# Optimization experiments

Measured on AMD Instinct MI355X. Metric: run time of the kernel, lower is better.

Reference implementation:

```python
import jax, jax.numpy as jnp
import numpy as np

K_HEADS = 8
D_HEAD = 64
D = K_HEADS * D_HEAD  # 512
B, TP, TQ, N = 8, 48, 48, 256


def setup_inputs() -> dict:
    key = jax.random.key(0)
    ks = jax.random.split(key, 13)
    s = 1.0 / np.sqrt(D)
    inp = {
        "X": jax.random.normal(ks[0], (B, TP, N, D), jnp.float32),
        "STE_P": jax.random.normal(ks[1], (B, TP, N, D), jnp.float32),
        "STE_Q": jax.random.normal(ks[2], (B, TQ, N, D), jnp.float32),
        "Wq": jax.random.uniform(ks[3], (D, D), jnp.float32, -s, s),
        "bq": jax.random.uniform(ks[4], (D,), jnp.float32, -s, s),
        "Wk": jax.random.uniform(ks[5], (D, D), jnp.float32, -s, s),
        "bk": jax.random.uniform(ks[6], (D,), jnp.float32, -s, s),
        "Wv": jax.random.uniform(ks[7], (D, D), jnp.float32, -s, s),
        "bv": jax.random.uniform(ks[8], (D,), jnp.float32, -s, s),
        "W1": jax.random.uniform(ks[9], (D, D), jnp.float32, -s, s),
        "b1": jax.random.uniform(ks[10], (D,), jnp.float32, -s, s),
        "W2": jax.random.uniform(ks[11], (D, D), jnp.float32, -s, s),
        "b2": jax.random.uniform(ks[12], (D,), jnp.float32, -s, s),
    }
    return inp


def reference(X, STE_P, STE_Q, Wq, bq, Wk, bk, Wv, bv, W1, b1, W2, b2):
    # ReLU-fused QKV projections
    q = jax.nn.relu(STE_Q @ Wq + bq)  # [B, Tq, N, D]
    k = jax.nn.relu(STE_P @ Wk + bk)  # [B, Tp, N, D]
    v = jax.nn.relu(X @ Wv + bv)      # [B, Tp, N, D]

    # split(last, d) + cat(dim 0) == introduce head axis h of size K
    b, tq, n, _ = q.shape
    tp = k.shape[1]
    q = q.reshape(b, tq, n, K_HEADS, D_HEAD)
    k = k.reshape(b, tp, n, K_HEADS, D_HEAD)
    v = v.reshape(b, tp, n, K_HEADS, D_HEAD)

    # attention over the TIME axis, per node and head: scores [b,h,n,tq,tp]
    scale = 1.0 / jnp.sqrt(jnp.asarray(D_HEAD, q.dtype))
    attn = jnp.einsum('bqnhd,bpnhd->bhnqp', q, k) * scale
    attn = jax.nn.softmax(attn, axis=-1)
    out = jnp.einsum('bhnqp,bpnhd->bqnhd', attn, v).reshape(b, tq, n, D)

    out = jax.nn.relu(out @ W1 + b1) @ W2 + b2
    return out
```

## Files before the change

kernel.cpp:

```cpp
#include <hip/hip_runtime.h>

typedef _Float16 f16;
typedef __fp16 hf2 __attribute__((ext_vector_type(2)));
typedef _Float16 f16x4 __attribute__((ext_vector_type(4)));
typedef _Float16 f16x8 __attribute__((ext_vector_type(8)));
typedef float f32x4 __attribute__((ext_vector_type(4)));

typedef const __attribute__((address_space(1))) unsigned int guint;
typedef __attribute__((address_space(3))) unsigned int luint;
__device__ __forceinline__ void gl_lds16(const void* g, void* l) {
    __builtin_amdgcn_global_load_lds((guint*)g, (luint*)l, 16, 0, 0);
}
template <int N>
__device__ __forceinline__ void vmwait() {
    if constexpr (N == 8)       asm volatile("s_waitcnt vmcnt(8)" ::: "memory");
    else if constexpr (N == 4)  asm volatile("s_waitcnt vmcnt(4)" ::: "memory");
    else                        asm volatile("s_waitcnt vmcnt(0)" ::: "memory");
}
__device__ __forceinline__ void barrier_raw() { __builtin_amdgcn_s_barrier(); __builtin_amdgcn_sched_barrier(0); }

__global__ __launch_bounds__(256) void wconv(const float* w0, const float* w1, const float* w2,
                                             const float* w3, const float* w4, f16* dst) {
    const float* src;
    switch (blockIdx.z) { case 0: src = w0; break; case 1: src = w1; break;
                          case 2: src = w2; break; case 3: src = w3; break; default: src = w4; }
    __shared__ float tile[32][33];
    int k0 = blockIdx.x * 32, n0 = blockIdx.y * 32;
    int t = threadIdx.x;
    int r = t >> 3, c4 = (t & 7) * 4;
    float4 v = *(const float4*)(src + (k0 + r) * 512 + n0 + c4);
    tile[r][c4 + 0] = v.x; tile[r][c4 + 1] = v.y; tile[r][c4 + 2] = v.z; tile[r][c4 + 3] = v.w;
    __syncthreads();
    f16x4 o;
    o[0] = (f16)tile[c4 + 0][r]; o[1] = (f16)tile[c4 + 1][r];
    o[2] = (f16)tile[c4 + 2][r]; o[3] = (f16)tile[c4 + 3][r];
    *(f16x4*)(dst + (size_t)blockIdx.z * 262144 + (n0 + r) * 512 + k0 + c4) = o;
}

template <bool A16, bool RELU, bool O16>
__global__ __launch_bounds__(512) void gemm_w8(const void* __restrict__ Ap,
                                               const f16* __restrict__ Bt,
                                               const float* __restrict__ bias,
                                               void* __restrict__ Cp) {
    constexpr int ASZ = A16 ? 16384 : 32768;
    constexpr int BSZ = 8192;
    constexpr int BUF = ASZ + BSZ;
    __shared__ __align__(16) char smem[2 * BUF];

    const int cpx = gridDim.x >> 3;
    const int orig = blockIdx.x;
    const int wgid = (orig & 7) * cpx + (orig >> 3);
    const int by = wgid & 3;
    const int bx = wgid >> 2;
    const int r0 = bx * 256, c0 = by * 128;

    const int t = threadIdx.x;
    const int j = t & 63, w = t >> 6;
    const int lr = j & 15, lq = j >> 4;
    const int wr = (w >> 1) * 64, wc = (w & 1) * 64;

    const char* aSrc;
    if (A16) aSrc = (const char*)Ap + ((size_t)(r0 + (t >> 2)) * 512 + ((t & 3) ^ ((t >> 3) & 3)) * 8) * 2;
    else     aSrc = (const char*)Ap + ((size_t)(r0 + (t >> 3)) * 512 + ((t & 7) ^ ((t >> 3) & 7)) * 4) * 4;
    const char* bSrc = (const char*)Bt + ((size_t)(c0 + (t >> 2)) * 512 + ((t & 3) ^ ((t >> 3) & 3)) * 8) * 2;

    int aoffL[4], aoffH[4], boff[4];
#pragma unroll
    for (int m = 0; m < 4; m++) {
        int row = wr + m * 16 + lr;
        if (A16) {
            aoffL[m] = row * 64 + ((lq ^ ((row >> 1) & 3)) << 4);
        } else {
            int s = row & 7;
            aoffL[m] = row * 128 + (((2 * lq) ^ s) << 4);
            aoffH[m] = row * 128 + (((2 * lq + 1) ^ s) << 4);
        }
    }
#pragma unroll
    for (int nb = 0; nb < 4; nb++) {
        int row = wc + nb * 16 + lr;
        boff[nb] = ASZ + row * 64 + ((lq ^ ((row >> 1) & 3)) << 4);
    }

    f32x4 acc[4][4] = {};

#define STAGE(tk, buf)                                                     \
    do {                                                                   \
        char* al_ = smem + (buf) * BUF + t * 16;                           \
        if (A16) {                                                         \
            const char* as_ = aSrc + (size_t)(tk) * 64;                    \
            gl_lds16(as_, al_);                                            \
            gl_lds16(as_ + 131072, al_ + 8192);                            \
        } else {                                                           \
            const char* as_ = aSrc + (size_t)(tk) * 128;                   \
            gl_lds16(as_, al_);                                            \
            gl_lds16(as_ + 131072, al_ + 8192);                            \
            gl_lds16(as_ + 262144, al_ + 16384);                           \
            gl_lds16(as_ + 393216, al_ + 24576);                           \
        }                                                                  \
        const char* bs_ = bSrc + (size_t)(tk) * 64;                        \
        gl_lds16(bs_, smem + (buf) * BUF + ASZ + t * 16);                  \
    } while (0)

#define COMPUTE(buf)                                                       \
    do {                                                                   \
        const char* sb_ = smem + (buf) * BUF;                              \
        f16x8 av[4], bv[4];                                                \
        _Pragma("unroll")                                                  \
        for (int m = 0; m < 4; m++) {                                      \
            if (A16) {                                                     \
                av[m] = *(const f16x8*)(sb_ + aoffL[m]);                   \
            } else {                                                       \
                float4 x0 = *(const float4*)(sb_ + aoffL[m]);              \
                float4 x1 = *(const float4*)(sb_ + aoffH[m]);              \
                hf2 p0 = __builtin_amdgcn_cvt_pkrtz(x0.x, x0.y);           \
                hf2 p1 = __builtin_amdgcn_cvt_pkrtz(x0.z, x0.w);           \
                hf2 p2 = __builtin_amdgcn_cvt_pkrtz(x1.x, x1.y);           \
                hf2 p3 = __builtin_amdgcn_cvt_pkrtz(x1.z, x1.w);           \
                f16x8 h;                                                   \
                h[0] = (f16)p0[0]; h[1] = (f16)p0[1]; h[2] = (f16)p1[0]; h[3] = (f16)p1[1]; \
                h[4] = (f16)p2[0]; h[5] = (f16)p2[1]; h[6] = (f16)p3[0]; h[7] = (f16)p3[1]; \
                av[m] = h;                                                 \
            }                                                              \
        }                                                                  \
        _Pragma("unroll")                                                  \
        for (int nb = 0; nb < 4; nb++) bv[nb] = *(const f16x8*)(sb_ + boff[nb]); \
        _Pragma("unroll")                                                  \
        for (int m = 0; m < 4; m++)                                        \
            _Pragma("unroll")                                              \
            for (int nb = 0; nb < 4; nb++)                                 \
                acc[m][nb] = __builtin_amdgcn_mfma_f32_16x16x32_f16(av[m], bv[nb], acc[m][nb], 0, 0, 0); \
    } while (0)

    STAGE(0, 0);
    __syncthreads();
    int cur = 0;
#pragma unroll 1
    for (int tk = 0; tk < 16; ++tk) {
        if (tk < 15) STAGE(tk + 1, cur ^ 1);
        COMPUTE(cur);
        __syncthreads();
        cur ^= 1;
    }
#undef STAGE
#undef COMPUTE

#pragma unroll
    for (int nb = 0; nb < 4; nb++) {
        int col = c0 + wc + nb * 16 + lr;
        float b = bias[col];
#pragma unroll
        for (int m = 0; m < 4; m++) {
#pragma unroll
            for (int r = 0; r < 4; r++) {
                float v = acc[m][nb][r] + b;
                if (RELU) v = fmaxf(v, 0.0f);
                size_t row = (size_t)(r0 + wr + m * 16 + lq * 4 + r);
                if (O16) ((f16*)Cp)[row * 512 + col] = (f16)v;
                else     ((float*)Cp)[row * 512 + col] = v;
            }
        }
    }
}

template <bool RELU, bool O16>
__global__ __launch_bounds__(512, 2) void gemm_8ph(const f16* __restrict__ A,
                                                   const f16* __restrict__ Bt,
                                                   const float* __restrict__ bias,
                                                   void* __restrict__ Cp) {
    constexpr int BUFSZ = 32768;
    __shared__ __align__(16) char smem[4 * BUFSZ];

    const int cpx = gridDim.x >> 3;
    const int orig = blockIdx.x;
    const int wgid = (orig & 7) * cpx + (orig >> 3);
    const int by = wgid & 1;
    const int bx = wgid >> 1;
    const int r0 = bx * 256, c0 = by * 256;

    const int t = threadIdx.x;
    const int j = t & 63, w = t >> 6;
    const int lr = j & 15, lq = j >> 4;
    const int wr = (w >> 2) * 128, wc = (w & 3) * 64;

    const int srow = t >> 2;
    const int sblk = (t & 3) ^ ((t >> 3) & 3);
    const f16* aS = A  + (size_t)(r0 + srow) * 512 + sblk * 8;
    const f16* bS = Bt + (size_t)(c0 + srow) * 512 + sblk * 8;
    const int dstT = t * 16;

    int aoff[8], boff[4];
#pragma unroll
    for (int m = 0; m < 8; m++) {
        int row = wr + m * 16 + lr;
        aoff[m] = row * 64 + ((lq ^ ((row >> 1) & 3)) << 4);
    }
#pragma unroll
    for (int nb = 0; nb < 4; nb++) {
        int row = wc + nb * 16 + lr;
        boff[nb] = 16384 + row * 64 + ((lq ^ ((row >> 1) & 3)) << 4);
    }

    f32x4 acc[8][4] = {};

    auto stageA = [&](int kt) {
        char* d = smem + (kt & 3) * BUFSZ + dstT;
        const f16* s = aS + kt * 32;
        gl_lds16(s, d);
        gl_lds16(s + 65536, d + 8192);
    };
    auto stageB = [&](int kt) {
        char* d = smem + (kt & 3) * BUFSZ + 16384 + dstT;
        const f16* s = bS + kt * 32;
        gl_lds16(s, d);
        gl_lds16(s + 65536, d + 8192);
    };

    stageA(0); stageB(0); stageA(1); stageB(1); stageA(2); stageB(2);

#pragma unroll 1
    for (int kt = 0; kt < 16; ++kt) {
        const char* sb = smem + (kt & 3) * BUFSZ;
        if (kt <= 13)      vmwait<8>();
        else if (kt == 14) vmwait<4>();
        else               vmwait<0>();
        barrier_raw();
        if (kt < 13) stageA(kt + 3);
        f16x8 bfr[4], afr[4];
#pragma unroll
        for (int nb = 0; nb < 4; nb++) bfr[nb] = *(const f16x8*)(sb + boff[nb]);
#pragma unroll
        for (int m = 0; m < 4; m++) afr[m] = *(const f16x8*)(sb + aoff[m]);
        __builtin_amdgcn_s_setprio(1);
#pragma unroll
        for (int m = 0; m < 4; m++)
#pragma unroll
            for (int nb = 0; nb < 4; nb++)
                acc[m][nb] = __builtin_amdgcn_mfma_f32_16x16x32_f16(afr[m], bfr[nb], acc[m][nb], 0, 0, 0);
        __builtin_amdgcn_s_setprio(0);
        barrier_raw();
        if (kt < 13) stageB(kt + 3);
        f16x8 afr2[4];
#pragma unroll
        for (int m = 0; m < 4; m++) afr2[m] = *(const f16x8*)(sb + aoff[m + 4]);
        __builtin_amdgcn_s_setprio(1);
#pragma unroll
        for (int m = 0; m < 4; m++)
#pragma unroll
            for (int nb = 0; nb < 4; nb++)
                acc[m + 4][nb] = __builtin_amdgcn_mfma_f32_16x16x32_f16(afr2[m], bfr[nb], acc[m + 4][nb], 0, 0, 0);
        __builtin_amdgcn_s_setprio(0);
    }

#pragma unroll
    for (int nb = 0; nb < 4; nb++) {
        int col = c0 + wc + nb * 16 + lr;
        float b = bias[col];
#pragma unroll
        for (int m = 0; m < 8; m++) {
#pragma unroll
            for (int r = 0; r < 4; r++) {
                float v = acc[m][nb][r] + b;
                if (RELU) v = fmaxf(v, 0.0f);
                size_t row = (size_t)(r0 + wr + m * 16 + lq * 4 + r);
                if (O16) ((f16*)Cp)[row * 512 + col] = (f16)v;
                else     ((float*)Cp)[row * 512 + col] = v;
            }
        }
    }
}

__global__ __launch_bounds__(64) void attn_kernel(const f16* __restrict__ q,
                                                  const f16* __restrict__ k,
                                                  const f16* __restrict__ v,
                                                  f16* __restrict__ out) {
    const int h = blockIdx.x, n = blockIdx.y, b = blockIdx.z;
    __shared__ f16 sQ[48 * 72];
    __shared__ f16 sK[48 * 72];
    __shared__ f16 sP[48 * 72];
    __shared__ f16 sVt[64 * 72];
    const int l = threadIdx.x, lr = l & 15, lq = l >> 4;
    const size_t rowstride = 256 * 512;
    const size_t base = ((size_t)(b * 48) * 256 + n) * 512 + h * 64;

    const int pr = l >> 3, pc = (l & 7) * 8;
#pragma unroll
    for (int pass = 0; pass < 6; pass++) {
        int row = pass * 8 + pr;
        size_t g = base + (size_t)row * rowstride + pc;
        f16x8 qv = *(const f16x8*)(q + g);
        f16x8 kv = *(const f16x8*)(k + g);
        f16x8 vv = *(const f16x8*)(v + g);
        *(f16x8*)&sQ[row * 72 + pc] = qv;
        *(f16x8*)&sK[row * 72 + pc] = kv;
#pragma unroll
        for (int jj = 0; jj < 8; jj++) sVt[(pc + jj) * 72 + row] = vv[jj];
    }
    {
        f16x8 z = {};
        *(f16x8*)&sVt[l * 72 + 48] = z;
        *(f16x8*)&sVt[l * 72 + 56] = z;
        if (l < 48) { *(f16x8*)&sP[l * 72 + 48] = z; *(f16x8*)&sP[l * 72 + 56] = z; }
    }
    __syncthreads();

    f32x4 s[3][3] = {};
#pragma unroll
    for (int ks = 0; ks < 2; ks++) {
        f16x8 aq[3], bk[3];
#pragma unroll
        for (int m = 0; m < 3; m++)  aq[m] = *(const f16x8*)&sQ[(m * 16 + lr) * 72 + ks * 32 + lq * 8];
#pragma unroll
        for (int nb = 0; nb < 3; nb++) bk[nb] = *(const f16x8*)&sK[(nb * 16 + lr) * 72 + ks * 32 + lq * 8];
#pragma unroll
        for (int m = 0; m < 3; m++)
#pragma unroll
            for (int nb = 0; nb < 3; nb++)
                s[m][nb] = __builtin_amdgcn_mfma_f32_16x16x32_f16(aq[m], bk[nb], s[m][nb], 0, 0, 0);
    }

#pragma unroll
    for (int m = 0; m < 3; m++) {
#pragma unroll
        for (int r = 0; r < 4; r++) {
            float a0 = s[m][0][r] * 0.125f, a1 = s[m][1][r] * 0.125f, a2 = s[m][2][r] * 0.125f;
            float mx = fmaxf(a0, fmaxf(a1, a2));
#pragma unroll
            for (int d = 1; d < 16; d <<= 1) mx = fmaxf(mx, __shfl_xor(mx, d));
            float e0 = __expf(a0 - mx), e1 = __expf(a1 - mx), e2 = __expf(a2 - mx);
            float sm = e0 + e1 + e2;
#pragma unroll
            for (int d = 1; d < 16; d <<= 1) sm += __shfl_xor(sm, d);
            float inv = 1.0f / sm;
            int row = m * 16 + lq * 4 + r;
            sP[row * 72 + 0  + lr] = (f16)(e0 * inv);
            sP[row * 72 + 16 + lr] = (f16)(e1 * inv);
            sP[row * 72 + 32 + lr] = (f16)(e2 * inv);
        }
    }
    __syncthreads();

    f32x4 o[3][4] = {};
#pragma unroll
    for (int ks = 0; ks < 2; ks++) {
        f16x8 ap[3], bvv[4];
#pragma unroll
        for (int m = 0; m < 3; m++)  ap[m] = *(const f16x8*)&sP[(m * 16 + lr) * 72 + ks * 32 + lq * 8];
#pragma unroll
        for (int nb = 0; nb < 4; nb++) bvv[nb] = *(const f16x8*)&sVt[(nb * 16 + lr) * 72 + ks * 32 + lq * 8];
#pragma unroll
        for (int m = 0; m < 3; m++)
#pragma unroll
            for (int nb = 0; nb < 4; nb++)
                o[m][nb] = __builtin_amdgcn_mfma_f32_16x16x32_f16(ap[m], bvv[nb], o[m][nb], 0, 0, 0);
    }

#pragma unroll
    for (int m = 0; m < 3; m++)
#pragma unroll
        for (int nb = 0; nb < 4; nb++)
#pragma unroll
            for (int r = 0; r < 4; r++) {
                int row = m * 16 + lq * 4 + r;
                out[base + (size_t)row * rowstride + nb * 16 + lr] = (f16)o[m][nb][r];
            }
}

extern "C" void kernel_launch(void* const* d_in, const int* in_sizes, int n_in,
                              void* d_out, int out_size, void* d_ws, size_t ws_size,
                              hipStream_t stream) {
    const float* X    = (const float*)d_in[0];
    const float* STEP = (const float*)d_in[1];
    const float* STEQ = (const float*)d_in[2];
    const float* Wq   = (const float*)d_in[3];
    const float* bq   = (const float*)d_in[4];
    const float* Wk   = (const float*)d_in[5];
    const float* bk   = (const float*)d_in[6];
    const float* Wv   = (const float*)d_in[7];
    const float* bv   = (const float*)d_in[8];
    const float* W1   = (const float*)d_in[9];
    const float* b1   = (const float*)d_in[10];
    const float* W2   = (const float*)d_in[11];
    const float* b2   = (const float*)d_in[12];
    float* out = (float*)d_out;

    const size_t MROWS = 98304;
    f16* ws  = (f16*)d_ws;
    f16* Wqt = ws;
    f16* Wkt = ws + 262144;
    f16* Wvt = ws + 524288;
    f16* W1t = ws + 786432;
    f16* W2t = ws + 1048576;
    f16* qb  = ws + 1310720;
    f16* kb  = qb + MROWS * 512;
    f16* vb  = kb + MROWS * 512;
    f16* attn = qb;
    f16* hb   = kb;

    wconv<<<dim3(16, 16, 5), 256, 0, stream>>>(Wq, Wk, Wv, W1, W2, ws);

    gemm_w8<false, true, true><<<1536, 512, 0, stream>>>(STEQ, Wqt, bq, qb);
    gemm_w8<false, true, true><<<1536, 512, 0, stream>>>(STEP, Wkt, bk, kb);
    gemm_w8<false, true, true><<<1536, 512, 0, stream>>>(X,    Wvt, bv, vb);

    attn_kernel<<<dim3(8, 256, 8), 64, 0, stream>>>(qb, kb, vb, attn);

    gemm_8ph<true,  true ><<<768, 512, 0, stream>>>(attn, W1t, b1, hb);
    gemm_8ph<false, false><<<768, 512, 0, stream>>>(hb,   W2t, b2, out);
}
```

Baseline: 620.3 us.

## Rewrite QKV projection GEMM with 256x256 tiles and triple-buffered staging

```diff
diff --git a/kernel.cpp b/kernel.cpp
--- a/kernel.cpp
+++ b/kernel.cpp
@@ -14,6 +14,7 @@
 template <int N>
 __device__ __forceinline__ void vmwait() {
     if constexpr (N == 8)       asm volatile("s_waitcnt vmcnt(8)" ::: "memory");
+    else if constexpr (N == 6)  asm volatile("s_waitcnt vmcnt(6)" ::: "memory");
     else if constexpr (N == 4)  asm volatile("s_waitcnt vmcnt(4)" ::: "memory");
     else                        asm volatile("s_waitcnt vmcnt(0)" ::: "memory");
 }
@@ -37,44 +38,37 @@
     *(f16x4*)(dst + (size_t)blockIdx.z * 262144 + (n0 + r) * 512 + k0 + c4) = o;
 }
 
-template <bool A16, bool RELU, bool O16>
-__global__ __launch_bounds__(512) void gemm_w8(const void* __restrict__ Ap,
-                                               const f16* __restrict__ Bt,
-                                               const float* __restrict__ bias,
-                                               void* __restrict__ Cp) {
-    constexpr int ASZ = A16 ? 16384 : 32768;
-    constexpr int BSZ = 8192;
-    constexpr int BUF = ASZ + BSZ;
-    __shared__ __align__(16) char smem[2 * BUF];
+__global__ __launch_bounds__(512, 1) void gemm_qkv(const float* __restrict__ A,
+                                                   const f16* __restrict__ Bt,
+                                                   const float* __restrict__ bias,
+                                                   f16* __restrict__ Cp) {
+    constexpr int ASZ = 32768;
+    constexpr int BUFSZ = ASZ + 16384;
+    __shared__ __align__(16) char smem[3 * BUFSZ];
 
     const int cpx = gridDim.x >> 3;
     const int orig = blockIdx.x;
     const int wgid = (orig & 7) * cpx + (orig >> 3);
-    const int by = wgid & 3;
-    const int bx = wgid >> 2;
-    const int r0 = bx * 256, c0 = by * 128;
+    const int by = wgid & 1;
+    const int bx = wgid >> 1;
+    const int r0 = bx * 256, c0 = by * 256;
 
     const int t = threadIdx.x;
     const int j = t & 63, w = t >> 6;
     const int lr = j & 15, lq = j >> 4;
-    const int wr = (w >> 1) * 64, wc = (w & 1) * 64;
-
-    const char* aSrc;
-    if (A16) aSrc = (const char*)Ap + ((size_t)(r0 + (t >> 2)) * 512 + ((t & 3) ^ ((t >> 3) & 3)) * 8) * 2;
-    else     aSrc = (const char*)Ap + ((size_t)(r0 + (t >> 3)) * 512 + ((t & 7) ^ ((t >> 3) & 7)) * 4) * 4;
-    const char* bSrc = (const char*)Bt + ((size_t)(c0 + (t >> 2)) * 512 + ((t & 3) ^ ((t >> 3) & 3)) * 8) * 2;
-
-    int aoffL[4], aoffH[4], boff[4];
-#pragma unroll
-    for (int m = 0; m < 4; m++) {
+    const int wr = (w >> 2) * 128, wc = (w & 3) * 64;
+
+    const float* aS = A + (size_t)(r0 + (t >> 3)) * 512 + ((t & 7) ^ ((t >> 3) & 7)) * 4;
+    const f16* bS = Bt + (size_t)(c0 + (t >> 2)) * 512 + ((t & 3) ^ ((t >> 3) & 3)) * 8;
+    const int dstT = t * 16;
+
+    int aoffL[8], aoffH[8], boff[4];
+#pragma unroll
+    for (int m = 0; m < 8; m++) {
         int row = wr + m * 16 + lr;
-        if (A16) {
-            aoffL[m] = row * 64 + ((lq ^ ((row >> 1) & 3)) << 4);
-        } else {
-            int s = row & 7;
-            aoffL[m] = row * 128 + (((2 * lq) ^ s) << 4);
-            aoffH[m] = row * 128 + (((2 * lq + 1) ^ s) << 4);
-        }
+        int s = row & 7;
+        aoffL[m] = row * 128 + (((2 * lq) ^ s) << 4);
+        aoffH[m] = row * 128 + (((2 * lq + 1) ^ s) << 4);
     }
 #pragma unroll
     for (int nb = 0; nb < 4; nb++) {
@@ -82,82 +76,84 @@
         boff[nb] = ASZ + row * 64 + ((lq ^ ((row >> 1) & 3)) << 4);
     }
 
-    f32x4 acc[4][4] = {};
-
-#define STAGE(tk, buf)                                                     \
-    do {                                                                   \
-        char* al_ = smem + (buf) * BUF + t * 16;                           \
-        if (A16) {                                                         \
-            const char* as_ = aSrc + (size_t)(tk) * 64;                    \
-            gl_lds16(as_, al_);                                            \
-            gl_lds16(as_ + 131072, al_ + 8192);                            \
-        } else {                                                           \
-            const char* as_ = aSrc + (size_t)(tk) * 128;                   \
-            gl_lds16(as_, al_);                                            \
-            gl_lds16(as_ + 131072, al_ + 8192);                            \
-            gl_lds16(as_ + 262144, al_ + 16384);                           \
-            gl_lds16(as_ + 393216, al_ + 24576);                           \
-        }                                                                  \
-        const char* bs_ = bSrc + (size_t)(tk) * 64;                        \
-        gl_lds16(bs_, smem + (buf) * BUF + ASZ + t * 16);                  \
-    } while (0)
-
-#define COMPUTE(buf)                                                       \
-    do {                                                                   \
-        const char* sb_ = smem + (buf) * BUF;                              \
-        f16x8 av[4], bv[4];                                                \
-        _Pragma("unroll")                                                  \
-        for (int m = 0; m < 4; m++) {                                      \
-            if (A16) {                                                     \
-                av[m] = *(const f16x8*)(sb_ + aoffL[m]);                   \
-            } else {                                                       \
-                float4 x0 = *(const float4*)(sb_ + aoffL[m]);              \
-                float4 x1 = *(const float4*)(sb_ + aoffH[m]);              \
-                hf2 p0 = __builtin_amdgcn_cvt_pkrtz(x0.x, x0.y);           \
-                hf2 p1 = __builtin_amdgcn_cvt_pkrtz(x0.z, x0.w);           \
-                hf2 p2 = __builtin_amdgcn_cvt_pkrtz(x1.x, x1.y);           \
-                hf2 p3 = __builtin_amdgcn_cvt_pkrtz(x1.z, x1.w);           \
-                f16x8 h;                                                   \
-                h[0] = (f16)p0[0]; h[1] = (f16)p0[1]; h[2] = (f16)p1[0]; h[3] = (f16)p1[1]; \
-                h[4] = (f16)p2[0]; h[5] = (f16)p2[1]; h[6] = (f16)p3[0]; h[7] = (f16)p3[1]; \
-                av[m] = h;                                                 \
-            }                                                              \
-        }                                                                  \
-        _Pragma("unroll")                                                  \
-        for (int nb = 0; nb < 4; nb++) bv[nb] = *(const f16x8*)(sb_ + boff[nb]); \
-        _Pragma("unroll")                                                  \
-        for (int m = 0; m < 4; m++)                                        \
-            _Pragma("unroll")                                              \
-            for (int nb = 0; nb < 4; nb++)                                 \
-                acc[m][nb] = __builtin_amdgcn_mfma_f32_16x16x32_f16(av[m], bv[nb], acc[m][nb], 0, 0, 0); \
-    } while (0)
-
-    STAGE(0, 0);
-    __syncthreads();
-    int cur = 0;
+    f32x4 acc[8][4] = {};
+
+    auto stageA = [&](int kt, int buf) {
+        char* d = smem + buf * BUFSZ + dstT;
+        const float* s = aS + kt * 32;
+#pragma unroll
+        for (int i = 0; i < 4; i++) gl_lds16(s + (size_t)i * 64 * 512, d + i * 8192);
+    };
+    auto stageB = [&](int kt, int buf) {
+        char* d = smem + buf * BUFSZ + ASZ + dstT;
+        const f16* s = bS + kt * 32;
+        gl_lds16(s, d);
+        gl_lds16(s + 65536, d + 8192);
+    };
+
+    auto loadA4 = [&](const char* sb, int m0, f16x8* afr) {
+#pragma unroll
+        for (int m = 0; m < 4; m++) {
+            float4 x0 = *(const float4*)(sb + aoffL[m0 + m]);
+            float4 x1 = *(const float4*)(sb + aoffH[m0 + m]);
+            hf2 p0 = __builtin_amdgcn_cvt_pkrtz(x0.x, x0.y);
+            hf2 p1 = __builtin_amdgcn_cvt_pkrtz(x0.z, x0.w);
+            hf2 p2 = __builtin_amdgcn_cvt_pkrtz(x1.x, x1.y);
+            hf2 p3 = __builtin_amdgcn_cvt_pkrtz(x1.z, x1.w);
+            f16x8 h;
+            h[0] = (f16)p0[0]; h[1] = (f16)p0[1]; h[2] = (f16)p1[0]; h[3] = (f16)p1[1];
+            h[4] = (f16)p2[0]; h[5] = (f16)p2[1]; h[6] = (f16)p3[0]; h[7] = (f16)p3[1];
+            afr[m] = h;
+        }
+    };
+
+    stageA(0, 0); stageB(0, 0); stageA(1, 1); stageB(1, 1);
+
+    int bufc = 0;
 #pragma unroll 1
-    for (int tk = 0; tk < 16; ++tk) {
-        if (tk < 15) STAGE(tk + 1, cur ^ 1);
-        COMPUTE(cur);
-        __syncthreads();
-        cur ^= 1;
-    }
-#undef STAGE
-#undef COMPUTE
+    for (int kt = 0; kt < 16; ++kt) {
+        const char* sb = smem + bufc * BUFSZ;
+        const int bufs = (bufc == 2) ? 0 : bufc + 1;
+        const int bufs2 = (bufs == 2) ? 0 : bufs + 1;
+        if (kt < 15) vmwait<6>(); else vmwait<0>();
+        barrier_raw();
+        if (kt < 14) stageA(kt + 2, bufs2);
+        f16x8 bfr[4], afr[4];
+#pragma unroll
+        for (int nb = 0; nb < 4; nb++) bfr[nb] = *(const f16x8*)(sb + boff[nb]);
+        loadA4(sb, 0, afr);
+        __builtin_amdgcn_s_setprio(1);
+#pragma unroll
+        for (int m = 0; m < 4; m++)
+#pragma unroll
+            for (int nb = 0; nb < 4; nb++)
+                acc[m][nb] = __builtin_amdgcn_mfma_f32_16x16x32_f16(afr[m], bfr[nb], acc[m][nb], 0, 0, 0);
+        __builtin_amdgcn_s_setprio(0);
+        barrier_raw();
+        if (kt < 14) stageB(kt + 2, bufs2);
+        f16x8 afr2[4];
+        loadA4(sb, 4, afr2);
+        __builtin_amdgcn_s_setprio(1);
+#pragma unroll
+        for (int m = 0; m < 4; m++)
+#pragma unroll
+            for (int nb = 0; nb < 4; nb++)
+                acc[m + 4][nb] = __builtin_amdgcn_mfma_f32_16x16x32_f16(afr2[m], bfr[nb], acc[m + 4][nb], 0, 0, 0);
+        __builtin_amdgcn_s_setprio(0);
+        bufc = bufs;
+    }
 
 #pragma unroll
     for (int nb = 0; nb < 4; nb++) {
         int col = c0 + wc + nb * 16 + lr;
         float b = bias[col];
 #pragma unroll
-        for (int m = 0; m < 4; m++) {
+        for (int m = 0; m < 8; m++) {
 #pragma unroll
             for (int r = 0; r < 4; r++) {
-                float v = acc[m][nb][r] + b;
-                if (RELU) v = fmaxf(v, 0.0f);
+                float v = fmaxf(acc[m][nb][r] + b, 0.0f);
                 size_t row = (size_t)(r0 + wr + m * 16 + lq * 4 + r);
-                if (O16) ((f16*)Cp)[row * 512 + col] = (f16)v;
-                else     ((float*)Cp)[row * 512 + col] = v;
+                Cp[row * 512 + col] = (f16)v;
             }
         }
     }
@@ -399,9 +395,9 @@
 
     wconv<<<dim3(16, 16, 5), 256, 0, stream>>>(Wq, Wk, Wv, W1, W2, ws);
 
-    gemm_w8<false, true, true><<<1536, 512, 0, stream>>>(STEQ, Wqt, bq, qb);
-    gemm_w8<false, true, true><<<1536, 512, 0, stream>>>(STEP, Wkt, bk, kb);
-    gemm_w8<false, true, true><<<1536, 512, 0, stream>>>(X,    Wvt, bv, vb);
+    gemm_qkv<<<768, 512, 0, stream>>>(STEQ, Wqt, bq, qb);
+    gemm_qkv<<<768, 512, 0, stream>>>(STEP, Wkt, bk, kb);
+    gemm_qkv<<<768, 512, 0, stream>>>(X,    Wvt, bv, vb);
 
     attn_kernel<<<dim3(8, 256, 8), 64, 0, stream>>>(qb, kb, vb, attn);
 
```

New measurement: 674.6 us. 1.09x slower.
